# Performance work log

Measured on AMD Instinct MI355X. Metric: run time of the kernel, lower is better.

The kernel has to match this reference:

```python
import jax, jax.numpy as jnp
from jax import lax
import numpy as np

B = 131072   # batch
M = 16       # in_channel (message dim, m=2^k with k=4)
NCH = 8      # n_channel (complex symbols)
CD = 16      # 2*n_channel
TAPS = 3     # rayleigh channel taps
R = 0.5      # code rate k/n
EBNO = 10.0 ** (7.0 / 10.0)
EPS = 1e-5


def setup_inputs() -> dict:
    ks = jax.random.split(jax.random.key(0), 48)
    f32 = jnp.float32
    def lin(i, o, n):
        return jax.random.normal(ks[i], (o, n), f32) / np.float32(np.sqrt(n))
    def cw(i, o, c, k):
        return jax.random.normal(ks[i], (o, c, k), f32) / np.float32(np.sqrt(c * k))
    def bv(i, n):
        return 0.01 * jax.random.normal(ks[i], (n,), f32)
    return dict(
        x=jax.random.normal(ks[0], (B, M), f32),
        noise=jax.random.normal(ks[1], (B, CD), f32) / np.float32(np.sqrt(2 * R * EBNO)),
        fading=jax.random.normal(ks[2], (B, TAPS, 2), f32),
        ew1=lin(3, M, M), eb1=bv(4, M),
        ew2=lin(5, CD, M), eb2=bv(6, CD),
        ec1w=cw(7, NCH, 1, 2), ec1b=bv(8, NCH),
        ec2w=cw(9, NCH, NCH, 4), ec2b=bv(10, NCH),
        ec3w=cw(11, NCH, NCH, 2), ec3b=bv(12, NCH),
        ec4w=cw(13, NCH, NCH, 2), ec4b=bv(14, NCH),
        ew3=lin(15, CD, 2 * CD), eb3=bv(16, CD),
        bng=jnp.ones((CD,), f32), bnb=jnp.zeros((CD,), f32),
        pw1=lin(17, 2 * CD, CD), pb1=bv(18, 2 * CD),
        pw2=lin(19, 4 * CD, 2 * CD), pb2=bv(20, 4 * CD),
        pw3=lin(21, CD // 2, 4 * CD), pb3=bv(22, CD // 2),
        pw4=lin(23, 2, CD // 2), pb4=bv(24, 2),
        dw1=lin(25, CD, CD), db1=bv(26, CD),
        dc1w=cw(27, NCH, 1, 2), dc1b=bv(28, NCH),
        dc2w=cw(29, NCH, NCH, 4), dc2b=bv(30, NCH),
        dc3w=cw(31, NCH, NCH, 2), dc3b=bv(32, NCH),
        dc4w=cw(33, NCH, NCH, 2), dc4b=bv(34, NCH),
        dw2=lin(35, CD, 2 * CD), db2=bv(36, CD),
        dw3=lin(37, CD, CD), db3=bv(38, CD),
        dw4=lin(39, M, CD), db4=bv(40, M),
    )


def _conv(h, w, bias, s):
    y = lax.conv_general_dilated(h, w, (s,), 'VALID', dimension_numbers=('NCH', 'OIH', 'NCH'))
    return y + bias[None, :, None]


def reference(x, noise, fading, ew1, eb1, ew2, eb2, ec1w, ec1b, ec2w, ec2b, ec3w, ec3b,
              ec4w, ec4b, ew3, eb3, bng, bnb, pw1, pb1, pw2, pb2, pw3, pb3, pw4, pb4,
              dw1, db1, dc1w, dc1b, dc2w, dc2b, dc3w, dc3b, dc4w, dc4b, dw2, db2,
              dw3, db3, dw4, db4):
    elu, tanh = jax.nn.elu, jnp.tanh
    Bn = x.shape[0]
    # ---- encoder ----
    h = elu(x @ ew1.T + eb1)
    h = elu(h @ ew2.T + eb2)                       # (B, CD)
    h = h[:, None, :]                              # (B, 1, CD)
    h = tanh(_conv(h, ec1w, ec1b, 1))              # (B, NCH, 15)
    h = tanh(_conv(h, ec2w, ec2b, 2))              # (B, NCH, 6)
    h = tanh(_conv(h, ec3w, ec3b, 1))              # (B, NCH, 5)
    h = tanh(_conv(h, ec4w, ec4b, 1))              # (B, NCH, 4)
    h = h.reshape(Bn, 2 * bng.shape[0])            # (B, 2*CD)
    h = h @ ew3.T + eb3                            # (B, CD)
    mu = h.mean(0)
    var = h.var(0)                                 # biased var (torch BN training mode)
    enc = (h - mu) / jnp.sqrt(var + EPS) * bng + bnb
    # ---- rayleigh multipath channel: vectorized complex FIR over taps ----
    taps = fading.shape[1]
    xc = enc.reshape(Bn, -1, 2)                    # (B, NCH, 2) re/im pairs
    n_sym = xc.shape[1]
    pad = taps - 1
    padded = jnp.pad(xc, ((0, 0), (pad, pad), (0, 0)))
    idx = jnp.arange(n_sym + taps - 1)[:, None] + jnp.arange(taps)[None, :]
    win = padded[:, idx]                           # (B, L_out, taps, 2)
    ff = fading[:, ::-1]                           # per-example flipped taps
    yr = jnp.einsum('blt,bt->bl', win[..., 0], ff[..., 0]) - jnp.einsum('blt,bt->bl', win[..., 1], ff[..., 1])
    yi = jnp.einsum('blt,bt->bl', win[..., 0], ff[..., 1]) + jnp.einsum('blt,bt->bl', win[..., 1], ff[..., 0])
    y = jnp.stack([yr, yi], -1)[:, :n_sym]         # drop trailing taps-1 samples
    c = y.reshape(Bn, 2 * n_sym) + noise
    # ---- channel parameter estimation ----
    p = elu(c @ pw1.T + pb1)
    p = tanh(p @ pw2.T + pb2)
    p = tanh(p @ pw3.T + pb3)
    hp = p @ pw4.T + pb4                           # (B, 2) estimated complex h
    # ---- transform: complex division x / h ----
    cc = c.reshape(Bn, n_sym, 2)
    hr, hi = hp[:, 0:1], hp[:, 1:2]
    den = hr * hr + hi * hi
    tr = (cc[..., 0] * hr + cc[..., 1] * hi) / den
    ti = (cc[..., 1] * hr - cc[..., 0] * hi) / den
    t = jnp.stack([tr, ti], -1).reshape(Bn, 2 * n_sym)
    # ---- decoder ----
    d = tanh(t @ dw1.T + db1)
    d = d[:, None, :]
    d = tanh(_conv(d, dc1w, dc1b, 1))
    d = tanh(_conv(d, dc2w, dc2b, 2))
    d = tanh(_conv(d, dc3w, dc3b, 1))
    d = tanh(_conv(d, dc4w, dc4b, 1))
    d = d.reshape(Bn, -1)
    d = tanh(d @ dw2.T + db2)
    d = tanh(d @ dw3.T + db3)
    return d @ dw4.T + db4
```

## Files before the change

### kernel.cpp

```cpp
#include <hip/hip_runtime.h>


#define BTOT 131072
#define NBLK 512
#define NW   6768

constexpr int EW1 = 0;     constexpr int EB1 = 256;
constexpr int EW2 = 272;   constexpr int EB2 = 528;
constexpr int EC1W = 544;  constexpr int EC1B = 560;
constexpr int EC2W = 568;  constexpr int EC2B = 824;
constexpr int EC3W = 832;  constexpr int EC3B = 960;
constexpr int EC4W = 968;  constexpr int EC4B = 1096;
constexpr int EW3 = 1104;  constexpr int EB3 = 1616;
constexpr int BNG = 1632;  constexpr int BNB = 1648;
constexpr int PW1 = 1664;  constexpr int PB1 = 2176;
constexpr int PW2 = 2208;  constexpr int PB2 = 4256;
constexpr int PW3 = 4320;  constexpr int PB3 = 4832;
constexpr int PW4 = 4840;  constexpr int PB4 = 4856;
constexpr int DW1 = 4864;  constexpr int DB1 = 5120;
constexpr int DC1W = 5136; constexpr int DC1B = 5152;
constexpr int DC2W = 5160; constexpr int DC2B = 5416;
constexpr int DC3W = 5424; constexpr int DC3B = 5552;
constexpr int DC4W = 5560; constexpr int DC4B = 5688;
constexpr int DW2 = 5696;  constexpr int DB2 = 6208;
constexpr int DW3 = 6224;  constexpr int DB3 = 6480;
constexpr int DW4 = 6496;  constexpr int DB4 = 6752;

constexpr size_t WS_W    = 0;
constexpr size_t WS_SC   = 28672;
constexpr size_t WS_PART = 32768;
constexpr size_t WS_HENC = 131072;
constexpr size_t WS_NEED_HENC = WS_HENC + (size_t)BTOT * 16 * 4;

__device__ __forceinline__ float bf2f(unsigned int u) {
  union { unsigned int i; float f; } v; v.i = u << 16; return v.f;
}
__device__ __forceinline__ unsigned short f2bf(float f) {
  union { float f; unsigned int i; } v; v.f = f;
  unsigned int x = v.i;
  return (unsigned short)((x + 0x7fffu + ((x >> 16) & 1u)) >> 16);
}
__device__ __forceinline__ void unpack8(uint4 u, float* f) {
  f[0] = bf2f(u.x & 0xffffu); f[1] = bf2f(u.x >> 16);
  f[2] = bf2f(u.y & 0xffffu); f[3] = bf2f(u.y >> 16);
  f[4] = bf2f(u.z & 0xffffu); f[5] = bf2f(u.z >> 16);
  f[6] = bf2f(u.w & 0xffffu); f[7] = bf2f(u.w >> 16);
}
__device__ __forceinline__ int sniff_bf16(const void* bng) {
  return *(const unsigned int*)bng != 0x3F800000u;
}
__device__ __forceinline__ void load16(const void* base, int b, int isbf, float* f) {
  if (isbf) {
    const uint4* p = (const uint4*)((const unsigned short*)base + (size_t)b * 16);
    unpack8(p[0], f); unpack8(p[1], f + 8);
  } else {
    const float4* p = (const float4*)((const float*)base + (size_t)b * 16);
#pragma unroll
    for (int q = 0; q < 4; q++) {
      float4 v = p[q];
      f[4 * q] = v.x; f[4 * q + 1] = v.y; f[4 * q + 2] = v.z; f[4 * q + 3] = v.w;
    }
  }
}
__device__ __forceinline__ float tanh_f(float x) {
  float e = __expf(2.0f * x);
  return 1.0f - 2.0f * __builtin_amdgcn_rcpf(e + 1.0f);
}
__device__ __forceinline__ float elu_f(float x) {
  return x > 0.0f ? x : __expf(x) - 1.0f;
}

template <int OUT, int IN, int WOFF, int BOFF, int ACT>
__device__ __forceinline__ void dense(const float* w, const float* in, float* out) {
#pragma unroll
  for (int m = 0; m < OUT; m++) {
    float v = w[BOFF + m];
#pragma unroll
    for (int k = 0; k < IN; k++) v += in[k] * w[WOFF + m * IN + k];
    if (ACT == 1) v = elu_f(v);
    if (ACT == 2) v = tanh_f(v);
    out[m] = v;
  }
}

template <int W1, int B1, int W2, int B2, int W3, int B3, int W4, int B4>
__device__ __forceinline__ void conv_chain(const float* w, const float h[16],
                                           float flat[32]) {
  float c1[4][8];
  float c2[6][8];
#pragma unroll
  for (int p = 0; p < 6; p++) {
    const int p0 = (p == 0) ? 0 : (2 * p + 2);
#pragma unroll
    for (int pos = p0; pos <= 2 * p + 3; ++pos) {
#pragma unroll
      for (int o = 0; o < 8; o++) {
        float v = w[W1 + o * 2] * h[pos] + w[W1 + o * 2 + 1] * h[pos + 1] + w[B1 + o];
        c1[pos & 3][o] = tanh_f(v);
      }
    }
#pragma unroll
    for (int o = 0; o < 8; o++) {
      float v = w[B2 + o];
#pragma unroll
      for (int k = 0; k < 4; k++) {
        const int pos = 2 * p + k;
#pragma unroll
        for (int i = 0; i < 8; i++) v += c1[pos & 3][i] * w[W2 + (o * 8 + i) * 4 + k];
      }
      c2[p][o] = tanh_f(v);
    }
  }
  float c3[5][8];
#pragma unroll
  for (int p = 0; p < 5; p++) {
#pragma unroll
    for (int o = 0; o < 8; o++) {
      float v = w[B3 + o];
#pragma unroll
      for (int i = 0; i < 8; i++)
        v += c2[p][i] * w[W3 + (o * 8 + i) * 2] + c2[p + 1][i] * w[W3 + (o * 8 + i) * 2 + 1];
      c3[p][o] = tanh_f(v);
    }
  }
#pragma unroll
  for (int p = 0; p < 4; p++) {
#pragma unroll
    for (int o = 0; o < 8; o++) {
      float v = w[B4 + o];
#pragma unroll
      for (int i = 0; i < 8; i++)
        v += c3[p][i] * w[W4 + (o * 8 + i) * 2] + c3[p + 1][i] * w[W4 + (o * 8 + i) * 2 + 1];
      flat[o * 4 + p] = tanh_f(v);
    }
  }
}

__device__ __forceinline__ void encoder(const void* __restrict__ x, int b, int isbf,
                                        const float* w, float he[16]) {
  float xv[16];
  load16(x, b, isbf, xv);
  float h1[16], h2[16];
  dense<16, 16, EW1, EB1, 1>(w, xv, h1);
  dense<16, 16, EW2, EB2, 1>(w, h1, h2);
  float flat[32];
  conv_chain<EC1W, EC1B, EC2W, EC2B, EC3W, EC3B, EC4W, EC4B>(w, h2, flat);
  dense<16, 32, EW3, EB3, 0>(w, flat, he);
}

struct Segs {
  const void* src[40];
  int cnt[40];
  int off[40];
};
__global__ __launch_bounds__(256) void k_convert(Segs s, const void* __restrict__ bng_src,
                                                 float* __restrict__ dst) {
  const int isbf = sniff_bf16(bng_src);
  const int seg = blockIdx.x;
  const int n = s.cnt[seg];
  const int o = s.off[seg];
  if (isbf) {
    const unsigned short* p = (const unsigned short*)s.src[seg];
    for (int i = threadIdx.x; i < n; i += 256) dst[o + i] = bf2f((unsigned int)p[i]);
  } else {
    const float* p = (const float*)s.src[seg];
    for (int i = threadIdx.x; i < n; i += 256) dst[o + i] = p[i];
  }
}

__global__ __launch_bounds__(256, 1) void k_enc(const void* __restrict__ x,
                                                const void* __restrict__ bng_src,
                                                const float* __restrict__ wg,
                                                float* __restrict__ partials,
                                                float* __restrict__ henc,
                                                int store_henc) {
  __shared__ float sw[NW];
  for (int i = threadIdx.x; i < NW / 4; i += 256)
    ((float4*)sw)[i] = ((const float4*)wg)[i];
  __syncthreads();

  const int isbf = sniff_bf16(bng_src);
  const int b = blockIdx.x * 256 + threadIdx.x;
  float he[16];
  encoder(x, b, isbf, sw, he);

  if (store_henc) {
    float4* hp = (float4*)(henc + (size_t)b * 16);
    hp[0] = make_float4(he[0], he[1], he[2], he[3]);
    hp[1] = make_float4(he[4], he[5], he[6], he[7]);
    hp[2] = make_float4(he[8], he[9], he[10], he[11]);
    hp[3] = make_float4(he[12], he[13], he[14], he[15]);
  }

  __shared__ float part[4][32];
  const int lane = threadIdx.x & 63;
  const int wid = threadIdx.x >> 6;
#pragma unroll
  for (int j = 0; j < 16; j++) {
    float s = he[j], q = he[j] * he[j];
#pragma unroll
    for (int m = 32; m >= 1; m >>= 1) {
      s += __shfl_xor(s, m, 64);
      q += __shfl_xor(q, m, 64);
    }
    if (lane == 0) { part[wid][j] = s; part[wid][16 + j] = q; }
  }
  __syncthreads();
  if (threadIdx.x < 32) {
    const int t = threadIdx.x;
    partials[blockIdx.x * 32 + t] = part[0][t] + part[1][t] + part[2][t] + part[3][t];
  }
}

__global__ __launch_bounds__(256) void k_red(const float* __restrict__ partials,
                                             const float* __restrict__ w,
                                             float* __restrict__ scsh) {
  __shared__ float red[8][32];
  __shared__ float tot[32];
  const int t = threadIdx.x;
  const int ch = t & 31, grp = t >> 5;
  float acc = 0.0f;
  for (int r = grp; r < NBLK; r += 8) acc += partials[r * 32 + ch];
  red[grp][ch] = acc;
  __syncthreads();
  if (t < 32) {
    float v = 0.0f;
#pragma unroll
    for (int g = 0; g < 8; g++) v += red[g][t];
    tot[t] = v;
  }
  __syncthreads();
  if (t < 16) {
    const float invB = 1.0f / (float)BTOT;
    float mu = tot[t] * invB;
    float var = tot[16 + t] * invB - mu * mu;
    float rstd = rsqrtf(var + 1e-5f);
    float sc = w[BNG + t] * rstd;
    scsh[t] = sc;
    scsh[16 + t] = w[BNB + t] - mu * sc;
  }
}

__global__ __launch_bounds__(256, 1) void k_main(const void* __restrict__ x,
                                                 const float* __restrict__ scsh,
                                                 const void* __restrict__ noise,
                                                 const void* __restrict__ fading,
                                                 const void* __restrict__ bng_src,
                                                 const float* __restrict__ wg,
                                                 const float* __restrict__ henc,
                                                 int use_henc,
                                                 void* __restrict__ out) {
  __shared__ float sw[NW];
  for (int i = threadIdx.x; i < NW / 4; i += 256)
    ((float4*)sw)[i] = ((const float4*)wg)[i];
  __syncthreads();

  const int isbf = sniff_bf16(bng_src);
  const int b = blockIdx.x * 256 + threadIdx.x;
  float enc[16];
  if (use_henc) {
    const float4* p = (const float4*)(henc + (size_t)b * 16);
#pragma unroll
    for (int q = 0; q < 4; q++) {
      float4 v = p[q];
      enc[4 * q] = v.x; enc[4 * q + 1] = v.y; enc[4 * q + 2] = v.z; enc[4 * q + 3] = v.w;
    }
  } else {
    encoder(x, b, isbf, sw, enc);
  }
  {
    const float* scp = scsh;
#pragma unroll
    for (int j = 0; j < 16; j++) enc[j] = enc[j] * scp[j] + scp[16 + j];
  }

  float fr[3], fi[3];
  if (isbf) {
    const unsigned int* fp =
        (const unsigned int*)((const unsigned short*)fading + (size_t)b * 6);
    unsigned int u0 = fp[0], u1 = fp[1], u2 = fp[2];
    fr[0] = bf2f(u0 & 0xffffu); fi[0] = bf2f(u0 >> 16);
    fr[1] = bf2f(u1 & 0xffffu); fi[1] = bf2f(u1 >> 16);
    fr[2] = bf2f(u2 & 0xffffu); fi[2] = bf2f(u2 >> 16);
  } else {
    const float2* fp = (const float2*)((const float*)fading + (size_t)b * 6);
    float2 a = fp[0], c2v = fp[1], d = fp[2];
    fr[0] = a.x; fi[0] = a.y; fr[1] = c2v.x; fi[1] = c2v.y; fr[2] = d.x; fi[2] = d.y;
  }
  float nz[16];
  load16(noise, b, isbf, nz);

  float c[16];
#pragma unroll
  for (int l = 0; l < 8; l++) {
    float ar = 0.0f, ai = 0.0f;
#pragma unroll
    for (int j = 0; j < 3; j++) {
      if (l - j >= 0) {
        float xr = enc[2 * (l - j)], xi = enc[2 * (l - j) + 1];
        ar += xr * fr[j] - xi * fi[j];
        ai += xr * fi[j] + xi * fr[j];
      }
    }
    c[2 * l] = ar + nz[2 * l];
    c[2 * l + 1] = ai + nz[2 * l + 1];
  }
  float p1[32];
  dense<32, 16, PW1, PB1, 1>(sw, c, p1);
  float p3[8];
#pragma unroll
  for (int j = 0; j < 8; j++) p3[j] = sw[PB3 + j];
#pragma unroll
  for (int n = 0; n < 64; n++) {
    float v = sw[PB2 + n];
#pragma unroll
    for (int k = 0; k < 32; k++) v += p1[k] * sw[PW2 + n * 32 + k];
    v = tanh_f(v);
#pragma unroll
    for (int j = 0; j < 8; j++) p3[j] += v * sw[PW3 + j * 64 + n];
  }
#pragma unroll
  for (int j = 0; j < 8; j++) p3[j] = tanh_f(p3[j]);
  float hr = sw[PB4 + 0], hi = sw[PB4 + 1];
#pragma unroll
  for (int k = 0; k < 8; k++) {
    hr += p3[k] * sw[PW4 + k];
    hi += p3[k] * sw[PW4 + 8 + k];
  }
  const float inv = __builtin_amdgcn_rcpf(hr * hr + hi * hi);
  float t[16];
#pragma unroll
  for (int l = 0; l < 8; l++) {
    float c0 = c[2 * l], c1 = c[2 * l + 1];
    t[2 * l] = (c0 * hr + c1 * hi) * inv;
    t[2 * l + 1] = (c1 * hr - c0 * hi) * inv;
  }
  float d1[16];
  dense<16, 16, DW1, DB1, 2>(sw, t, d1);
  float flat[32];
  conv_chain<DC1W, DC1B, DC2W, DC2B, DC3W, DC3B, DC4W, DC4B>(sw, d1, flat);
  float d2[16], d3[16], o[16];
  dense<16, 32, DW2, DB2, 2>(sw, flat, d2);
  dense<16, 16, DW3, DB3, 2>(sw, d2, d3);
  dense<16, 16, DW4, DB4, 0>(sw, d3, o);

  if (isbf) {
    unsigned int ov[8];
#pragma unroll
    for (int j = 0; j < 8; j++)
      ov[j] = (unsigned int)f2bf(o[2 * j]) | ((unsigned int)f2bf(o[2 * j + 1]) << 16);
    uint4* op = (uint4*)((unsigned short*)out + (size_t)b * 16);
    op[0] = make_uint4(ov[0], ov[1], ov[2], ov[3]);
    op[1] = make_uint4(ov[4], ov[5], ov[6], ov[7]);
  } else {
    float4* op = (float4*)((float*)out + (size_t)b * 16);
#pragma unroll
    for (int q = 0; q < 4; q++)
      op[q] = make_float4(o[4 * q], o[4 * q + 1], o[4 * q + 2], o[4 * q + 3]);
  }
}

extern "C" void kernel_launch(void* const* d_in, const int* in_sizes, int n_in,
                              void* d_out, int out_size, void* d_ws, size_t ws_size,
                              hipStream_t stream) {
  float* wbuf = (float*)((char*)d_ws + WS_W);
  float* scsh = (float*)((char*)d_ws + WS_SC);
  float* partials = (float*)((char*)d_ws + WS_PART);
  float* henc = (float*)((char*)d_ws + WS_HENC);
  const int use_henc = (ws_size >= WS_NEED_HENC) ? 1 : 0;

  static const int offs[40] = {
      EW1, EB1, EW2, EB2, EC1W, EC1B, EC2W, EC2B, EC3W, EC3B, EC4W, EC4B,
      EW3, EB3, BNG, BNB, PW1, PB1, PW2, PB2, PW3, PB3, PW4, PB4,
      DW1, DB1, DC1W, DC1B, DC2W, DC2B, DC3W, DC3B, DC4W, DC4B,
      DW2, DB2, DW3, DB3, DW4, DB4};
  Segs segs;
  for (int k = 0; k < 40; k++) {
    segs.src[k] = d_in[3 + k];
    segs.cnt[k] = in_sizes[3 + k];
    segs.off[k] = offs[k];
  }
  const void* bng_src = d_in[17];
  k_convert<<<40, 256, 0, stream>>>(segs, bng_src, wbuf);
  k_enc<<<NBLK, 256, 0, stream>>>(d_in[0], bng_src, wbuf, partials, henc, use_henc);
  k_red<<<1, 256, 0, stream>>>(partials, wbuf, scsh);
  k_main<<<NBLK, 256, 0, stream>>>(d_in[0], scsh, d_in[1], d_in[2], bng_src, wbuf,
                                   henc, use_henc, d_out);
}
```

Before: 292.6 us.

## Process two batch rows per thread with packed float2 math

Each thread now handles two samples (t and t+65536) using 2-wide float vectors, so the compiler can emit packed FP32 FMA instructions, and every weight read from LDS is shared by both samples. Weight reads are widened to float2/float4 LDS loads. The block size drops to 128 threads with the same 512 blocks, which halves the thread count and doubles register pressure per thread. That risks spills and leaves 512 blocks of two waves each to cover the GPU's latency.

```diff
diff --git a/kernel.cpp b/kernel.cpp
--- a/kernel.cpp
+++ b/kernel.cpp
@@ -2,8 +2,12 @@
 
 
 #define BTOT 131072
+#define NT2  65536
+#define BLK  128
 #define NBLK 512
 #define NW   6768
+
+typedef float v2 __attribute__((ext_vector_type(2)));
 
 constexpr int EW1 = 0;     constexpr int EB1 = 256;
 constexpr int EW2 = 272;   constexpr int EB2 = 528;
@@ -32,6 +36,7 @@
 constexpr size_t WS_HENC = 131072;
 constexpr size_t WS_NEED_HENC = WS_HENC + (size_t)BTOT * 16 * 4;
 
+__device__ __forceinline__ v2 sp(float s) { v2 r; r.x = s; r.y = s; return r; }
 __device__ __forceinline__ float bf2f(unsigned int u) {
   union { unsigned int i; float f; } v; v.i = u << 16; return v.f;
 }
@@ -62,32 +67,50 @@
     }
   }
 }
+__device__ __forceinline__ void load16_2(const void* base, int bA, int bB, int isbf,
+                                         v2* f) {
+  float a[16], b[16];
+  load16(base, bA, isbf, a);
+  load16(base, bB, isbf, b);
+#pragma unroll
+  for (int j = 0; j < 16; j++) { f[j].x = a[j]; f[j].y = b[j]; }
+}
 __device__ __forceinline__ float tanh_f(float x) {
   float e = __expf(2.0f * x);
   return 1.0f - 2.0f * __builtin_amdgcn_rcpf(e + 1.0f);
 }
-__device__ __forceinline__ float elu_f(float x) {
-  return x > 0.0f ? x : __expf(x) - 1.0f;
+__device__ __forceinline__ v2 tanh_v(v2 x) {
+  v2 r; r.x = tanh_f(x.x); r.y = tanh_f(x.y); return r;
+}
+__device__ __forceinline__ v2 elu_v(v2 x) {
+  v2 r;
+  r.x = x.x > 0.0f ? x.x : __expf(x.x) - 1.0f;
+  r.y = x.y > 0.0f ? x.y : __expf(x.y) - 1.0f;
+  return r;
 }
 
 template <int OUT, int IN, int WOFF, int BOFF, int ACT>
-__device__ __forceinline__ void dense(const float* w, const float* in, float* out) {
+__device__ __forceinline__ void dense2(const float* w, const v2* in, v2* out) {
 #pragma unroll
   for (int m = 0; m < OUT; m++) {
-    float v = w[BOFF + m];
-#pragma unroll
-    for (int k = 0; k < IN; k++) v += in[k] * w[WOFF + m * IN + k];
-    if (ACT == 1) v = elu_f(v);
-    if (ACT == 2) v = tanh_f(v);
+    v2 v = sp(w[BOFF + m]);
+#pragma unroll
+    for (int k = 0; k < IN; k += 4) {
+      float4 wv = *(const float4*)(w + WOFF + m * IN + k);
+      v += in[k] * wv.x; v += in[k + 1] * wv.y;
+      v += in[k + 2] * wv.z; v += in[k + 3] * wv.w;
+    }
+    if (ACT == 1) v = elu_v(v);
+    if (ACT == 2) v = tanh_v(v);
     out[m] = v;
   }
 }
 
 template <int W1, int B1, int W2, int B2, int W3, int B3, int W4, int B4>
-__device__ __forceinline__ void conv_chain(const float* w, const float h[16],
-                                           float flat[32]) {
-  float c1[4][8];
-  float c2[6][8];
+__device__ __forceinline__ void conv_chain2(const float* w, const v2 h[16],
+                                            v2 flat[32]) {
+  v2 c1[4][8];
+  v2 c2[6][8];
 #pragma unroll
   for (int p = 0; p < 6; p++) {
     const int p0 = (p == 0) ? 0 : (2 * p + 2);
@@ -95,57 +118,64 @@
     for (int pos = p0; pos <= 2 * p + 3; ++pos) {
 #pragma unroll
       for (int o = 0; o < 8; o++) {
-        float v = w[W1 + o * 2] * h[pos] + w[W1 + o * 2 + 1] * h[pos + 1] + w[B1 + o];
-        c1[pos & 3][o] = tanh_f(v);
+        float2 wv = *(const float2*)(w + W1 + o * 2);
+        v2 v = h[pos] * wv.x + h[pos + 1] * wv.y + sp(w[B1 + o]);
+        c1[pos & 3][o] = tanh_v(v);
       }
     }
 #pragma unroll
     for (int o = 0; o < 8; o++) {
-      float v = w[B2 + o];
-#pragma unroll
-      for (int k = 0; k < 4; k++) {
-        const int pos = 2 * p + k;
-#pragma unroll
-        for (int i = 0; i < 8; i++) v += c1[pos & 3][i] * w[W2 + (o * 8 + i) * 4 + k];
-      }
-      c2[p][o] = tanh_f(v);
-    }
-  }
-  float c3[5][8];
+      v2 v = sp(w[B2 + o]);
+#pragma unroll
+      for (int i = 0; i < 8; i++) {
+        float4 wv = *(const float4*)(w + W2 + (o * 8 + i) * 4);
+        v += c1[(2 * p) & 3][i] * wv.x;
+        v += c1[(2 * p + 1) & 3][i] * wv.y;
+        v += c1[(2 * p + 2) & 3][i] * wv.z;
+        v += c1[(2 * p + 3) & 3][i] * wv.w;
+      }
+      c2[p][o] = tanh_v(v);
+    }
+  }
+  v2 c3[5][8];
 #pragma unroll
   for (int p = 0; p < 5; p++) {
 #pragma unroll
     for (int o = 0; o < 8; o++) {
-      float v = w[B3 + o];
-#pragma unroll
-      for (int i = 0; i < 8; i++)
-        v += c2[p][i] * w[W3 + (o * 8 + i) * 2] + c2[p + 1][i] * w[W3 + (o * 8 + i) * 2 + 1];
-      c3[p][o] = tanh_f(v);
+      v2 v = sp(w[B3 + o]);
+#pragma unroll
+      for (int i = 0; i < 8; i++) {
+        float2 wv = *(const float2*)(w + W3 + (o * 8 + i) * 2);
+        v += c2[p][i] * wv.x + c2[p + 1][i] * wv.y;
+      }
+      c3[p][o] = tanh_v(v);
     }
   }
 #pragma unroll
   for (int p = 0; p < 4; p++) {
 #pragma unroll
     for (int o = 0; o < 8; o++) {
-      float v = w[B4 + o];
-#pragma unroll
-      for (int i = 0; i < 8; i++)
-        v += c3[p][i] * w[W4 + (o * 8 + i) * 2] + c3[p + 1][i] * w[W4 + (o * 8 + i) * 2 + 1];
-      flat[o * 4 + p] = tanh_f(v);
-    }
-  }
-}
-
-__device__ __forceinline__ void encoder(const void* __restrict__ x, int b, int isbf,
-                                        const float* w, float he[16]) {
-  float xv[16];
-  load16(x, b, isbf, xv);
-  float h1[16], h2[16];
-  dense<16, 16, EW1, EB1, 1>(w, xv, h1);
-  dense<16, 16, EW2, EB2, 1>(w, h1, h2);
-  float flat[32];
-  conv_chain<EC1W, EC1B, EC2W, EC2B, EC3W, EC3B, EC4W, EC4B>(w, h2, flat);
-  dense<16, 32, EW3, EB3, 0>(w, flat, he);
+      v2 v = sp(w[B4 + o]);
+#pragma unroll
+      for (int i = 0; i < 8; i++) {
+        float2 wv = *(const float2*)(w + W4 + (o * 8 + i) * 2);
+        v += c3[p][i] * wv.x + c3[p + 1][i] * wv.y;
+      }
+      flat[o * 4 + p] = tanh_v(v);
+    }
+  }
+}
+
+__device__ __forceinline__ void encoder2(const void* __restrict__ x, int bA, int bB,
+                                         int isbf, const float* w, v2 he[16]) {
+  v2 xv[16];
+  load16_2(x, bA, bB, isbf, xv);
+  v2 h1[16], h2[16];
+  dense2<16, 16, EW1, EB1, 1>(w, xv, h1);
+  dense2<16, 16, EW2, EB2, 1>(w, h1, h2);
+  v2 flat[32];
+  conv_chain2<EC1W, EC1B, EC2W, EC2B, EC3W, EC3B, EC4W, EC4B>(w, h2, flat);
+  dense2<16, 32, EW3, EB3, 0>(w, flat, he);
 }
 
 struct Segs {
@@ -168,36 +198,40 @@
   }
 }
 
-__global__ __launch_bounds__(256, 1) void k_enc(const void* __restrict__ x,
+__global__ __launch_bounds__(BLK, 1) void k_enc(const void* __restrict__ x,
                                                 const void* __restrict__ bng_src,
                                                 const float* __restrict__ wg,
                                                 float* __restrict__ partials,
                                                 float* __restrict__ henc,
                                                 int store_henc) {
   __shared__ float sw[NW];
-  for (int i = threadIdx.x; i < NW / 4; i += 256)
+  for (int i = threadIdx.x; i < NW / 4; i += BLK)
     ((float4*)sw)[i] = ((const float4*)wg)[i];
   __syncthreads();
 
   const int isbf = sniff_bf16(bng_src);
-  const int b = blockIdx.x * 256 + threadIdx.x;
-  float he[16];
-  encoder(x, b, isbf, sw, he);
+  const int t = blockIdx.x * BLK + threadIdx.x;
+  const int bA = t, bB = t + NT2;
+  v2 he[16];
+  encoder2(x, bA, bB, isbf, sw, he);
 
   if (store_henc) {
-    float4* hp = (float4*)(henc + (size_t)b * 16);
-    hp[0] = make_float4(he[0], he[1], he[2], he[3]);
-    hp[1] = make_float4(he[4], he[5], he[6], he[7]);
-    hp[2] = make_float4(he[8], he[9], he[10], he[11]);
-    hp[3] = make_float4(he[12], he[13], he[14], he[15]);
-  }
-
-  __shared__ float part[4][32];
+    float4* ha = (float4*)(henc + (size_t)bA * 16);
+    float4* hb = (float4*)(henc + (size_t)bB * 16);
+#pragma unroll
+    for (int q = 0; q < 4; q++) {
+      ha[q] = make_float4(he[4 * q].x, he[4 * q + 1].x, he[4 * q + 2].x, he[4 * q + 3].x);
+      hb[q] = make_float4(he[4 * q].y, he[4 * q + 1].y, he[4 * q + 2].y, he[4 * q + 3].y);
+    }
+  }
+
+  __shared__ float part[2][32];
   const int lane = threadIdx.x & 63;
   const int wid = threadIdx.x >> 6;
 #pragma unroll
   for (int j = 0; j < 16; j++) {
-    float s = he[j], q = he[j] * he[j];
+    float s = he[j].x + he[j].y;
+    float q = he[j].x * he[j].x + he[j].y * he[j].y;
 #pragma unroll
     for (int m = 32; m >= 1; m >>= 1) {
       s += __shfl_xor(s, m, 64);
@@ -207,8 +241,8 @@
   }
   __syncthreads();
   if (threadIdx.x < 32) {
-    const int t = threadIdx.x;
-    partials[blockIdx.x * 32 + t] = part[0][t] + part[1][t] + part[2][t] + part[3][t];
+    const int i = threadIdx.x;
+    partials[blockIdx.x * 32 + i] = part[0][i] + part[1][i];
   }
 }
 
@@ -241,7 +275,7 @@
   }
 }
 
-__global__ __launch_bounds__(256, 1) void k_main(const void* __restrict__ x,
+__global__ __launch_bounds__(BLK, 1) void k_main(const void* __restrict__ x,
                                                  const float* __restrict__ scsh,
                                                  const void* __restrict__ noise,
                                                  const void* __restrict__ fading,
@@ -251,53 +285,64 @@
                                                  int use_henc,
                                                  void* __restrict__ out) {
   __shared__ float sw[NW];
-  for (int i = threadIdx.x; i < NW / 4; i += 256)
+  for (int i = threadIdx.x; i < NW / 4; i += BLK)
     ((float4*)sw)[i] = ((const float4*)wg)[i];
   __syncthreads();
 
   const int isbf = sniff_bf16(bng_src);
-  const int b = blockIdx.x * 256 + threadIdx.x;
-  float enc[16];
+  const int t = blockIdx.x * BLK + threadIdx.x;
+  const int bA = t, bB = t + NT2;
+  v2 enc[16];
   if (use_henc) {
-    const float4* p = (const float4*)(henc + (size_t)b * 16);
+    const float4* pa = (const float4*)(henc + (size_t)bA * 16);
+    const float4* pb = (const float4*)(henc + (size_t)bB * 16);
 #pragma unroll
     for (int q = 0; q < 4; q++) {
-      float4 v = p[q];
-      enc[4 * q] = v.x; enc[4 * q + 1] = v.y; enc[4 * q + 2] = v.z; enc[4 * q + 3] = v.w;
+      float4 a = pa[q], b = pb[q];
+      enc[4 * q].x = a.x; enc[4 * q].y = b.x;
+      enc[4 * q + 1].x = a.y; enc[4 * q + 1].y = b.y;
+      enc[4 * q + 2].x = a.z; enc[4 * q + 2].y = b.z;
+      enc[4 * q + 3].x = a.w; enc[4 * q + 3].y = b.w;
     }
   } else {
-    encoder(x, b, isbf, sw, enc);
-  }
-  {
-    const float* scp = scsh;
-#pragma unroll
-    for (int j = 0; j < 16; j++) enc[j] = enc[j] * scp[j] + scp[16 + j];
-  }
-
-  float fr[3], fi[3];
+    encoder2(x, bA, bB, isbf, sw, enc);
+  }
+#pragma unroll
+  for (int j = 0; j < 16; j++) enc[j] = enc[j] * scsh[j] + sp(scsh[16 + j]);
+
+  v2 fr[3], fi[3];
   if (isbf) {
-    const unsigned int* fp =
-        (const unsigned int*)((const unsigned short*)fading + (size_t)b * 6);
-    unsigned int u0 = fp[0], u1 = fp[1], u2 = fp[2];
-    fr[0] = bf2f(u0 & 0xffffu); fi[0] = bf2f(u0 >> 16);
-    fr[1] = bf2f(u1 & 0xffffu); fi[1] = bf2f(u1 >> 16);
-    fr[2] = bf2f(u2 & 0xffffu); fi[2] = bf2f(u2 >> 16);
+    const unsigned int* fa =
+        (const unsigned int*)((const unsigned short*)fading + (size_t)bA * 6);
+    const unsigned int* fb =
+        (const unsigned int*)((const unsigned short*)fading + (size_t)bB * 6);
+#pragma unroll
+    for (int j = 0; j < 3; j++) {
+      unsigned int ua = fa[j], ub = fb[j];
+      fr[j].x = bf2f(ua & 0xffffu); fi[j].x = bf2f(ua >> 16);
+      fr[j].y = bf2f(ub & 0xffffu); fi[j].y = bf2f(ub >> 16);
+    }
   } else {
-    const float2* fp = (const float2*)((const float*)fading + (size_t)b * 6);
-    float2 a = fp[0], c2v = fp[1], d = fp[2];
-    fr[0] = a.x; fi[0] = a.y; fr[1] = c2v.x; fi[1] = c2v.y; fr[2] = d.x; fi[2] = d.y;
-  }
-  float nz[16];
-  load16(noise, b, isbf, nz);
-
-  float c[16];
+    const float2* fa = (const float2*)((const float*)fading + (size_t)bA * 6);
+    const float2* fb = (const float2*)((const float*)fading + (size_t)bB * 6);
+#pragma unroll
+    for (int j = 0; j < 3; j++) {
+      float2 a = fa[j], b = fb[j];
+      fr[j].x = a.x; fi[j].x = a.y;
+      fr[j].y = b.x; fi[j].y = b.y;
+    }
+  }
+  v2 nz[16];
+  load16_2(noise, bA, bB, isbf, nz);
+
+  v2 c[16];
 #pragma unroll
   for (int l = 0; l < 8; l++) {
-    float ar = 0.0f, ai = 0.0f;
+    v2 ar = sp(0.0f), ai = sp(0.0f);
 #pragma unroll
     for (int j = 0; j < 3; j++) {
       if (l - j >= 0) {
-        float xr = enc[2 * (l - j)], xi = enc[2 * (l - j) + 1];
+        v2 xr = enc[2 * (l - j)], xi = enc[2 * (l - j) + 1];
         ar += xr * fr[j] - xi * fi[j];
         ai += xr * fi[j] + xi * fr[j];
       }
@@ -305,58 +350,79 @@
     c[2 * l] = ar + nz[2 * l];
     c[2 * l + 1] = ai + nz[2 * l + 1];
   }
-  float p1[32];
-  dense<32, 16, PW1, PB1, 1>(sw, c, p1);
-  float p3[8];
-#pragma unroll
-  for (int j = 0; j < 8; j++) p3[j] = sw[PB3 + j];
-#pragma unroll
-  for (int n = 0; n < 64; n++) {
-    float v = sw[PB2 + n];
-#pragma unroll
-    for (int k = 0; k < 32; k++) v += p1[k] * sw[PW2 + n * 32 + k];
-    v = tanh_f(v);
-#pragma unroll
-    for (int j = 0; j < 8; j++) p3[j] += v * sw[PW3 + j * 64 + n];
-  }
-#pragma unroll
-  for (int j = 0; j < 8; j++) p3[j] = tanh_f(p3[j]);
-  float hr = sw[PB4 + 0], hi = sw[PB4 + 1];
+  v2 p1[32];
+  dense2<32, 16, PW1, PB1, 1>(sw, c, p1);
+  v2 p3[8];
+#pragma unroll
+  for (int j = 0; j < 8; j++) p3[j] = sp(sw[PB3 + j]);
+#pragma unroll
+  for (int n0 = 0; n0 < 64; n0 += 4) {
+    v2 tv[4];
+#pragma unroll
+    for (int u = 0; u < 4; u++) {
+      const int n = n0 + u;
+      v2 v = sp(sw[PB2 + n]);
+#pragma unroll
+      for (int k = 0; k < 32; k += 4) {
+        float4 wv = *(const float4*)(sw + PW2 + n * 32 + k);
+        v += p1[k] * wv.x; v += p1[k + 1] * wv.y;
+        v += p1[k + 2] * wv.z; v += p1[k + 3] * wv.w;
+      }
+      tv[u] = tanh_v(v);
+    }
+#pragma unroll
+    for (int j = 0; j < 8; j++) {
+      float4 wv = *(const float4*)(sw + PW3 + j * 64 + n0);
+      p3[j] += tv[0] * wv.x + tv[1] * wv.y + tv[2] * wv.z + tv[3] * wv.w;
+    }
+  }
+#pragma unroll
+  for (int j = 0; j < 8; j++) p3[j] = tanh_v(p3[j]);
+  v2 hr = sp(sw[PB4 + 0]), hi = sp(sw[PB4 + 1]);
 #pragma unroll
   for (int k = 0; k < 8; k++) {
     hr += p3[k] * sw[PW4 + k];
     hi += p3[k] * sw[PW4 + 8 + k];
   }
-  const float inv = __builtin_amdgcn_rcpf(hr * hr + hi * hi);
-  float t[16];
+  v2 den = hr * hr + hi * hi;
+  v2 inv; inv.x = __builtin_amdgcn_rcpf(den.x); inv.y = __builtin_amdgcn_rcpf(den.y);
+  v2 tt[16];
 #pragma unroll
   for (int l = 0; l < 8; l++) {
-    float c0 = c[2 * l], c1 = c[2 * l + 1];
-    t[2 * l] = (c0 * hr + c1 * hi) * inv;
-    t[2 * l + 1] = (c1 * hr - c0 * hi) * inv;
-  }
-  float d1[16];
-  dense<16, 16, DW1, DB1, 2>(sw, t, d1);
-  float flat[32];
-  conv_chain<DC1W, DC1B, DC2W, DC2B, DC3W, DC3B, DC4W, DC4B>(sw, d1, flat);
-  float d2[16], d3[16], o[16];
-  dense<16, 32, DW2, DB2, 2>(sw, flat, d2);
-  dense<16, 16, DW3, DB3, 2>(sw, d2, d3);
-  dense<16, 16, DW4, DB4, 0>(sw, d3, o);
+    v2 c0 = c[2 * l], c1v = c[2 * l + 1];
+    tt[2 * l] = (c0 * hr + c1v * hi) * inv;
+    tt[2 * l + 1] = (c1v * hr - c0 * hi) * inv;
+  }
+  v2 d1[16];
+  dense2<16, 16, DW1, DB1, 2>(sw, tt, d1);
+  v2 flat[32];
+  conv_chain2<DC1W, DC1B, DC2W, DC2B, DC3W, DC3B, DC4W, DC4B>(sw, d1, flat);
+  v2 d2[16], d3[16], o[16];
+  dense2<16, 32, DW2, DB2, 2>(sw, flat, d2);
+  dense2<16, 16, DW3, DB3, 2>(sw, d2, d3);
+  dense2<16, 16, DW4, DB4, 0>(sw, d3, o);
 
   if (isbf) {
-    unsigned int ov[8];
-#pragma unroll
-    for (int j = 0; j < 8; j++)
-      ov[j] = (unsigned int)f2bf(o[2 * j]) | ((unsigned int)f2bf(o[2 * j + 1]) << 16);
-    uint4* op = (uint4*)((unsigned short*)out + (size_t)b * 16);
-    op[0] = make_uint4(ov[0], ov[1], ov[2], ov[3]);
-    op[1] = make_uint4(ov[4], ov[5], ov[6], ov[7]);
+    unsigned int ovA[8], ovB[8];
+#pragma unroll
+    for (int j = 0; j < 8; j++) {
+      ovA[j] = (unsigned int)f2bf(o[2 * j].x) | ((unsigned int)f2bf(o[2 * j + 1].x) << 16);
+      ovB[j] = (unsigned int)f2bf(o[2 * j].y) | ((unsigned int)f2bf(o[2 * j + 1].y) << 16);
+    }
+    uint4* oa = (uint4*)((unsigned short*)out + (size_t)bA * 16);
+    uint4* ob = (uint4*)((unsigned short*)out + (size_t)bB * 16);
+    oa[0] = make_uint4(ovA[0], ovA[1], ovA[2], ovA[3]);
+    oa[1] = make_uint4(ovA[4], ovA[5], ovA[6], ovA[7]);
+    ob[0] = make_uint4(ovB[0], ovB[1], ovB[2], ovB[3]);
+    ob[1] = make_uint4(ovB[4], ovB[5], ovB[6], ovB[7]);
   } else {
-    float4* op = (float4*)((float*)out + (size_t)b * 16);
-#pragma unroll
-    for (int q = 0; q < 4; q++)
-      op[q] = make_float4(o[4 * q], o[4 * q + 1], o[4 * q + 2], o[4 * q + 3]);
+    float4* oa = (float4*)((float*)out + (size_t)bA * 16);
+    float4* ob = (float4*)((float*)out + (size_t)bB * 16);
+#pragma unroll
+    for (int q = 0; q < 4; q++) {
+      oa[q] = make_float4(o[4 * q].x, o[4 * q + 1].x, o[4 * q + 2].x, o[4 * q + 3].x);
+      ob[q] = make_float4(o[4 * q].y, o[4 * q + 1].y, o[4 * q + 2].y, o[4 * q + 3].y);
+    }
   }
 }
 
@@ -382,8 +448,8 @@
   }
   const void* bng_src = d_in[17];
   k_convert<<<40, 256, 0, stream>>>(segs, bng_src, wbuf);
-  k_enc<<<NBLK, 256, 0, stream>>>(d_in[0], bng_src, wbuf, partials, henc, use_henc);
+  k_enc<<<NBLK, BLK, 0, stream>>>(d_in[0], bng_src, wbuf, partials, henc, use_henc);
   k_red<<<1, 256, 0, stream>>>(partials, wbuf, scsh);
-  k_main<<<NBLK, 256, 0, stream>>>(d_in[0], scsh, d_in[1], d_in[2], bng_src, wbuf,
+  k_main<<<NBLK, BLK, 0, stream>>>(d_in[0], scsh, d_in[1], d_in[2], bng_src, wbuf,
                                    henc, use_henc, d_out);
 }
```

New measurement: 258.4 us. -11.7%, faster.
